# Performance work log

Hardware: AMD Instinct MI355X
Metric: run time of the kernel (lower is better)

Reference implementation:

```python
import jax, jax.numpy as jnp
import numpy as np

N_NODES = 100000
N_EDGES = 1600000
DIM_IN, DIM_H, DIM_OUT = 15, 128, 1


def _glorot(key, shape):
    fan_in, fan_out = shape[0], shape[1]
    lim = float(np.sqrt(6.0 / (fan_in + fan_out)))
    return jax.random.uniform(key, shape, jnp.float32, -lim, lim)


def setup_inputs() -> dict:
    key = jax.random.key(0)
    ks = jax.random.split(key, 12)
    x = jax.random.normal(ks[0], (N_NODES, DIM_IN), jnp.float32)
    edge_index = jax.random.randint(ks[1], (2, N_EDGES), 0, N_NODES, jnp.int64)
    # PyG SAGEConv: out = lin_l(mean_aggr(x_src)) + lin_r(x_dst); bias lives in lin_l.
    # Weights stored as [in, out] for x @ W.
    params = {
        "W1l": _glorot(ks[2], (DIM_IN, DIM_H)), "W1r": _glorot(ks[3], (DIM_IN, DIM_H)), "b1": jnp.zeros((DIM_H,), jnp.float32),
        "W2l": _glorot(ks[4], (DIM_H, DIM_H)), "W2r": _glorot(ks[5], (DIM_H, DIM_H)), "b2": jnp.zeros((DIM_H,), jnp.float32),
        "W3l": _glorot(ks[6], (DIM_H, DIM_OUT)), "W3r": _glorot(ks[7], (DIM_H, DIM_OUT)), "b3": jnp.zeros((DIM_OUT,), jnp.float32),
    }
    return {"x": x, "edge_index": edge_index, **params}


def _sage_conv(h, src, dst, deg_inv, Wl, Wr, b):
    # mean-aggregate source features at destination nodes
    agg = jax.ops.segment_sum(h[src], dst, num_segments=N_NODES) * deg_inv
    return agg @ Wl + h @ Wr + b


def reference(x, edge_index, W1l, W1r, b1, W2l, W2r, b2, W3l, W3r, b3):
    src, dst = edge_index[0], edge_index[1]
    deg = jax.ops.segment_sum(jnp.ones((src.shape[0],), x.dtype), dst, num_segments=N_NODES)
    deg_inv = (1.0 / jnp.maximum(deg, 1.0))[:, None]  # [N,1]
    h = jax.nn.relu(_sage_conv(x, src, dst, deg_inv, W1l, W1r, b1))  # dropout is identity in eval
    h = jax.nn.relu(_sage_conv(h, src, dst, deg_inv, W2l, W2r, b2))
    h = _sage_conv(h, src, dst, deg_inv, W3l, W3r, b3)
    return h
```

## Files before the change

kernel.cpp:

```cpp
#include <hip/hip_runtime.h>
#include <hip/hip_bf16.h>

constexpr int N = 100000;
constexpr int E = 1600000;
constexpr int DIN = 15;
constexpr int DH  = 128;
constexpr int K2  = 256;
constexpr int NPAD = 100032;

constexpr int CHUNK     = 8192;
constexpr int NBLK_P1   = (E + CHUNK - 1) / CHUNK;
constexpr int BKT_NODES = 512;
constexpr int NBKT      = (N + BKT_NODES - 1) / BKT_NODES;
constexpr int LREC_CAP  = 10240;

constexpr int PREP_IDS    = DH * K2 + NPAD * 8 + DH * 32 + (NPAD - N) * 8;
constexpr int PREP_BLOCKS = (PREP_IDS + 1023) / 1024;

typedef short short8 __attribute__((ext_vector_type(8)));
typedef float f32x4  __attribute__((ext_vector_type(4)));

__device__ __forceinline__ unsigned short f2bf_rne(float f) {
    unsigned u = __float_as_uint(f);
    u += 0x7fffu + ((u >> 16) & 1u);
    return (unsigned short)(u >> 16);
}
__device__ __forceinline__ float bf2f(unsigned short h) {
    return __uint_as_float(((unsigned)h) << 16);
}
__device__ __forceinline__ float bflo(unsigned u) { return __uint_as_float(u << 16); }
__device__ __forceinline__ float bfhi(unsigned u) { return __uint_as_float(u & 0xffff0000u); }

__global__ __launch_bounds__(1024) void k_pre(const int* __restrict__ src,
                                              const int* __restrict__ dst,
                                              unsigned int* __restrict__ bsorted,
                                              int* __restrict__ offg,
                                              int* __restrict__ btot,
                                              const float* __restrict__ x,
                                              const float* __restrict__ W2l,
                                              const float* __restrict__ W2r,
                                              const float* __restrict__ W1l,
                                              const float* __restrict__ W1r,
                                              unsigned int* __restrict__ xb32,
                                              unsigned short* __restrict__ Wthi,
                                              unsigned short* __restrict__ Wtlo,
                                              unsigned short* __restrict__ Wt1hi,
                                              unsigned short* __restrict__ Wt1lo,
                                              unsigned int* __restrict__ agg1b) {
    __shared__ int hist[256];
    __shared__ int scn[256];
    __shared__ int fill[256];
    __shared__ unsigned int srt[CHUNK];
    const int t = threadIdx.x;

    if (blockIdx.x >= NBLK_P1) {
        int id = (blockIdx.x - NBLK_P1) * 1024 + t;
        if (id < DH * K2) {
            int col = id & 127;
            int k   = id >> 7;
            float wv = (k < DH) ? W2l[k * DH + col] : W2r[(k - DH) * DH + col];
            unsigned short hi = f2bf_rne(wv);
            unsigned short lo = f2bf_rne(wv - bf2f(hi));
            Wthi[col * K2 + k] = hi;
            Wtlo[col * K2 + k] = lo;
            return;
        }
        int xid = id - DH * K2;
        if (xid < NPAD * 8) {
            int n = xid >> 3, d2 = xid & 7;
            unsigned v = 0;
            if (n < N) {
                int d0 = 2 * d2, d1 = 2 * d2 + 1;
                float v0 = x[n * DIN + d0];
                float v1 = (d1 < DIN) ? x[n * DIN + d1] : 0.f;
                v = (unsigned)f2bf_rne(v0) | ((unsigned)f2bf_rne(v1) << 16);
            }
            xb32[xid] = v;
            return;
        }
        int wid = xid - NPAD * 8;
        if (wid < DH * 32) {
            int col = wid >> 5;
            int k   = wid & 31;
            float wv = 0.f;
            if (k < DIN)                 wv = W1l[k * DH + col];
            else if (k >= 16 && k < 31)  wv = W1r[(k - 16) * DH + col];
            unsigned short hi = f2bf_rne(wv);
            unsigned short lo = f2bf_rne(wv - bf2f(hi));
            Wt1hi[col * 32 + k] = hi;
            Wt1lo[col * 32 + k] = lo;
            return;
        }
        int aid = wid - DH * 32;
        if (aid < (NPAD - N) * 8) agg1b[N * 8 + aid] = 0;
        return;
    }

    const int blk = blockIdx.x;
    const int e0  = blk * CHUNK;
    if (t < 256) hist[t] = 0;
    __syncthreads();
#pragma unroll
    for (int j = 0; j < CHUNK / 1024; ++j) {
        int i = e0 + t + j * 1024;
        if (i < E) atomicAdd(&hist[dst[i] >> 9], 1);
    }
    __syncthreads();
    if (t < 256) {
        if (t < NBKT && hist[t]) atomicAdd(&btot[t], hist[t]);
        scn[t] = hist[t];
    }
    __syncthreads();
    for (int d = 1; d < 256; d <<= 1) {
        int v = (t >= d && t < 256) ? scn[t - d] : 0;
        __syncthreads();
        if (t < 256) scn[t] += v;
        __syncthreads();
    }
    if (t < 256) {
        int excl = (t == 0) ? 0 : scn[t - 1];
        fill[t] = excl;
        if (t < NBKT) offg[blk * (NBKT + 1) + t] = excl;
        if (t == 0)   offg[blk * (NBKT + 1) + NBKT] = scn[NBKT - 1];
    }
    __syncthreads();
#pragma unroll
    for (int j = 0; j < CHUNK / 1024; ++j) {
        int i = e0 + t + j * 1024;
        if (i < E) {
            int dv = dst[i];
            int b  = dv >> 9;
            int pos = atomicAdd(&fill[b], 1);
            srt[pos] = ((unsigned)(dv & 511) << 17) | (unsigned)src[i];
        }
    }
    __syncthreads();
    for (int i = t; i < CHUNK; i += 1024) bsorted[e0 + i] = srt[i];
}

__global__ __launch_bounds__(1024) void k_p2(const unsigned int* __restrict__ bsorted,
                                             const int* __restrict__ offg,
                                             const int* __restrict__ btot,
                                             int* __restrict__ csr,
                                             int* __restrict__ rowptr,
                                             float* __restrict__ deg_inv) {
    __shared__ unsigned int lrec[LREC_CAP];
    __shared__ int cum[NBLK_P1 + 1];
    __shared__ int runstart[NBLK_P1];
    __shared__ int ldeg[BKT_NODES];
    __shared__ int lrp[BKT_NODES];
    __shared__ int lfill[BKT_NODES];
    __shared__ int pscan[256];
    __shared__ int sbs;

    const int b = blockIdx.x;
    const int t = threadIdx.x;

    if (t < 256) pscan[t] = (t < NBKT) ? btot[t] : 0;
    __syncthreads();
    for (int d = 1; d < 256; d <<= 1) {
        int v = (t >= d && t < 256) ? pscan[t - d] : 0;
        __syncthreads();
        if (t < 256) pscan[t] += v;
        __syncthreads();
    }
    if (t == 0) sbs = (b == 0) ? 0 : pscan[b - 1];
    __syncthreads();
    const int bs = sbs;

    int cnt_blk = 0;
    if (t < NBLK_P1) {
        int o0 = offg[t * (NBKT + 1) + b];
        cnt_blk = offg[t * (NBKT + 1) + b + 1] - o0;
        runstart[t] = o0;
    }
    __syncthreads();
    if (t < 256) pscan[t] = cnt_blk;
    __syncthreads();
    for (int d = 1; d < 256; d <<= 1) {
        int v = (t >= d && t < 256) ? pscan[t - d] : 0;
        __syncthreads();
        if (t < 256) pscan[t] += v;
        __syncthreads();
    }
    if (t < NBLK_P1) cum[t] = (t == 0) ? 0 : pscan[t - 1];
    if (t == 0) cum[NBLK_P1] = pscan[NBLK_P1 - 1];
    if (t < BKT_NODES) ldeg[t] = 0;
    __syncthreads();

    int total = cum[NBLK_P1];
    if (total > LREC_CAP) total = LREC_CAP;

    for (int i = t; i < total; i += 1024) {
        int lo = 0, hi = NBLK_P1;
        while (hi - lo > 1) {
            int mid = (lo + hi) >> 1;
            if (cum[mid] <= i) lo = mid; else hi = mid;
        }
        lrec[i] = bsorted[lo * CHUNK + runstart[lo] + (i - cum[lo])];
    }
    __syncthreads();

    for (int i = t; i < total; i += 1024) atomicAdd(&ldeg[lrec[i] >> 17], 1);
    __syncthreads();

    int p0 = 0, p1 = 0;
    if (t < 256) {
        p0 = ldeg[2 * t];
        p1 = ldeg[2 * t + 1];
        pscan[t] = p0 + p1;
    }
    __syncthreads();
    for (int d = 1; d < 256; d <<= 1) {
        int v = (t >= d && t < 256) ? pscan[t - d] : 0;
        __syncthreads();
        if (t < 256) pscan[t] += v;
        __syncthreads();
    }
    if (t < 256) {
        int pairbase = (t == 0) ? 0 : pscan[t - 1];
        lrp[2 * t]     = pairbase;
        lrp[2 * t + 1] = pairbase + p0;
    }
    if (t < BKT_NODES) lfill[t] = 0;
    __syncthreads();

    for (int i = t; i < total; i += 1024) {
        unsigned rec = lrec[i];
        int ld  = rec >> 17;
        int pos = lrp[ld] + atomicAdd(&lfill[ld], 1);
        csr[bs + pos] = (int)(rec & 0x1ffff);
    }
    if (t < BKT_NODES) {
        int g = b * BKT_NODES + t;
        if (g < N) {
            rowptr[g]  = bs + lrp[t];
            deg_inv[g] = 1.0f / fmaxf((float)ldeg[t], 1.0f);
        }
    }
    if (b == NBKT - 1 && t == 0) rowptr[N] = E;
}

__global__ __launch_bounds__(256) void k_agg1(const int* __restrict__ rowptr,
                                              const int* __restrict__ csr,
                                              const uint2* __restrict__ xb2,
                                              const float* __restrict__ deg_inv,
                                              uint2* __restrict__ agg1b2) {
    const int tid = threadIdx.x;
    const int l4  = tid & 3;
    const int gb4 = (tid & 63) & 60;
    const int n = blockIdx.x * 64 + (tid >> 2);
    if (n >= N) return;
    const int lo = rowptr[n], hi = rowptr[n + 1];
    float a0 = 0.f, a1 = 0.f, a2 = 0.f, a3 = 0.f;
    float b0 = 0.f, b1 = 0.f, b2 = 0.f, b3 = 0.f;
    float c0 = 0.f, c1 = 0.f, c2 = 0.f, c3 = 0.f;
    float d0 = 0.f, d1 = 0.f, d2 = 0.f, d3 = 0.f;
    int base = lo;
    for (; base + 8 <= hi; base += 8) {
        int e0 = csr[base + l4];
        int e1 = csr[base + 4 + l4];
        int s0 = __shfl(e0, gb4 + 0), s1 = __shfl(e0, gb4 + 1);
        int s2 = __shfl(e0, gb4 + 2), s3 = __shfl(e0, gb4 + 3);
        int s4 = __shfl(e1, gb4 + 0), s5 = __shfl(e1, gb4 + 1);
        int s6 = __shfl(e1, gb4 + 2), s7 = __shfl(e1, gb4 + 3);
        uint2 u0 = xb2[s0 * 4 + l4];
        uint2 u1 = xb2[s1 * 4 + l4];
        uint2 u2 = xb2[s2 * 4 + l4];
        uint2 u3 = xb2[s3 * 4 + l4];
        uint2 u4 = xb2[s4 * 4 + l4];
        uint2 u5 = xb2[s5 * 4 + l4];
        uint2 u6 = xb2[s6 * 4 + l4];
        uint2 u7 = xb2[s7 * 4 + l4];
        a0 += bflo(u0.x); a1 += bfhi(u0.x); a2 += bflo(u0.y); a3 += bfhi(u0.y);
        b0 += bflo(u1.x); b1 += bfhi(u1.x); b2 += bflo(u1.y); b3 += bfhi(u1.y);
        c0 += bflo(u2.x); c1 += bfhi(u2.x); c2 += bflo(u2.y); c3 += bfhi(u2.y);
        d0 += bflo(u3.x); d1 += bfhi(u3.x); d2 += bflo(u3.y); d3 += bfhi(u3.y);
        a0 += bflo(u4.x); a1 += bfhi(u4.x); a2 += bflo(u4.y); a3 += bfhi(u4.y);
        b0 += bflo(u5.x); b1 += bfhi(u5.x); b2 += bflo(u5.y); b3 += bfhi(u5.y);
        c0 += bflo(u6.x); c1 += bfhi(u6.x); c2 += bflo(u6.y); c3 += bfhi(u6.y);
        d0 += bflo(u7.x); d1 += bfhi(u7.x); d2 += bflo(u7.y); d3 += bfhi(u7.y);
    }
    int cnt = hi - base;
    if (cnt > 0) {
        int e0 = (base + l4 < hi) ? csr[base + l4] : 0;
        int e1 = (base + 4 + l4 < hi) ? csr[base + 4 + l4] : 0;
        int jm = min(cnt, 4);
        for (int j = 0; j < jm; ++j) {
            int s = __shfl(e0, gb4 + j);
            uint2 u = xb2[s * 4 + l4];
            a0 += bflo(u.x); a1 += bfhi(u.x); a2 += bflo(u.y); a3 += bfhi(u.y);
        }
        for (int j = 4; j < cnt; ++j) {
            int s = __shfl(e1, gb4 + j - 4);
            uint2 u = xb2[s * 4 + l4];
            b0 += bflo(u.x); b1 += bfhi(u.x); b2 += bflo(u.y); b3 += bfhi(u.y);
        }
    }
    const float di = deg_inv[n];
    float v0 = ((a0 + b0) + (c0 + d0)) * di;
    float v1 = ((a1 + b1) + (c1 + d1)) * di;
    float v2 = ((a2 + b2) + (c2 + d2)) * di;
    float v3 = ((a3 + b3) + (c3 + d3)) * di;
    uint2 o;
    o.x = (unsigned)f2bf_rne(v0) | ((unsigned)f2bf_rne(v1) << 16);
    o.y = (unsigned)f2bf_rne(v2) | ((unsigned)f2bf_rne(v3) << 16);
    agg1b2[n * 4 + l4] = o;
}

__global__ __launch_bounds__(256) void k_h1(const uint4* __restrict__ agg1b4,
                                            const uint4* __restrict__ xb4,
                                            const unsigned short* __restrict__ Wt1hi,
                                            const unsigned short* __restrict__ Wt1lo,
                                            const float* __restrict__ b1,
                                            unsigned int* __restrict__ h1hi32) {
    __shared__ __align__(16) unsigned short sA[4 * 64 * 8];
    __shared__ __align__(16) unsigned short sH[64 * 128];
    __shared__ float sb[DH];

    const int tid   = threadIdx.x;
    const int node0 = blockIdx.x * 64;

    if (tid < DH) sb[tid] = b1[tid];
    {
        int c = tid >> 6;
        int n = tid & 63;
        uint4 v = (c < 2) ? agg1b4[(node0 + n) * 2 + c]
                          : xb4[(node0 + n) * 2 + (c - 2)];
        *(uint4*)&sA[(c * 64 + (n ^ c)) * 8] = v;
    }
    __syncthreads();

    const int w    = tid >> 6;
    const int lane = tid & 63;
    const int cg   = lane & 15;
    const int lg   = lane >> 4;

    f32x4 acc[4][2];
#pragma unroll
    for (int a = 0; a < 4; ++a)
#pragma unroll
        for (int b = 0; b < 2; ++b)
            acc[a][b] = (f32x4){0.f, 0.f, 0.f, 0.f};

    short8 bh0 = *(const short8*)&Wt1hi[(w * 32 + 0 * 16 + cg) * 32 + lg * 8];
    short8 bh1 = *(const short8*)&Wt1hi[(w * 32 + 1 * 16 + cg) * 32 + lg * 8];
    short8 bl0 = *(const short8*)&Wt1lo[(w * 32 + 0 * 16 + cg) * 32 + lg * 8];
    short8 bl1 = *(const short8*)&Wt1lo[(w * 32 + 1 * 16 + cg) * 32 + lg * 8];

#pragma unroll
    for (int rt = 0; rt < 4; ++rt) {
        const int n = rt * 16 + cg;
        short8 a = *(const short8*)&sA[(lg * 64 + (n ^ lg)) * 8];
        acc[rt][0] = __builtin_amdgcn_mfma_f32_16x16x32_bf16(a, bh0, acc[rt][0], 0, 0, 0);
        acc[rt][0] = __builtin_amdgcn_mfma_f32_16x16x32_bf16(a, bl0, acc[rt][0], 0, 0, 0);
        acc[rt][1] = __builtin_amdgcn_mfma_f32_16x16x32_bf16(a, bh1, acc[rt][1], 0, 0, 0);
        acc[rt][1] = __builtin_amdgcn_mfma_f32_16x16x32_bf16(a, bl1, acc[rt][1], 0, 0, 0);
    }

#pragma unroll
    for (int rt = 0; rt < 4; ++rt)
#pragma unroll
        for (int ci = 0; ci < 2; ++ci) {
            const int col = w * 32 + ci * 16 + cg;
            const float bb = sb[col];
#pragma unroll
            for (int reg = 0; reg < 4; ++reg) {
                const int row = rt * 16 + lg * 4 + reg;
                sH[row * 128 + col] = f2bf_rne(fmaxf(acc[rt][ci][reg] + bb, 0.f));
            }
        }
    __syncthreads();
    const uint4* sH4 = (const uint4*)sH;
    uint4* out4 = (uint4*)h1hi32;
#pragma unroll
    for (int it = 0; it < 4; ++it) {
        int idx = tid + it * 256;
        out4[node0 * 16 + idx] = sH4[idx];
    }
}

__global__ __launch_bounds__(256) void k_agg2(const int* __restrict__ rowptr,
                                              const int* __restrict__ csr,
                                              const unsigned int* __restrict__ h1b,
                                              const float* __restrict__ deg_inv,
                                              unsigned int* __restrict__ agg2b) {
    const int lane = threadIdx.x & 63;
    const int n = blockIdx.x * 4 + (threadIdx.x >> 6);
    if (n >= N) return;
    const int lo = rowptr[n], hi = rowptr[n + 1];
    float a0x = 0.f, a0y = 0.f, a1x = 0.f, a1y = 0.f;
    float a2x = 0.f, a2y = 0.f, a3x = 0.f, a3y = 0.f;
    float a4x = 0.f, a4y = 0.f, a5x = 0.f, a5y = 0.f;
    float a6x = 0.f, a6y = 0.f, a7x = 0.f, a7y = 0.f;
    for (int base = lo; base < hi; base += 64) {
        const int cnt = min(64, hi - base);
        int e = (base + lane < hi) ? csr[base + lane] : 0;
        int j = 0;
        for (; j + 8 <= cnt; j += 8) {
            int s0 = __shfl(e, j + 0), s1 = __shfl(e, j + 1);
            int s2 = __shfl(e, j + 2), s3 = __shfl(e, j + 3);
            int s4 = __shfl(e, j + 4), s5 = __shfl(e, j + 5);
            int s6 = __shfl(e, j + 6), s7 = __shfl(e, j + 7);
            unsigned u0 = h1b[s0 * 64 + lane];
            unsigned u1 = h1b[s1 * 64 + lane];
            unsigned u2 = h1b[s2 * 64 + lane];
            unsigned u3 = h1b[s3 * 64 + lane];
            unsigned u4 = h1b[s4 * 64 + lane];
            unsigned u5 = h1b[s5 * 64 + lane];
            unsigned u6 = h1b[s6 * 64 + lane];
            unsigned u7 = h1b[s7 * 64 + lane];
            a0x += bflo(u0); a0y += bfhi(u0);
            a1x += bflo(u1); a1y += bfhi(u1);
            a2x += bflo(u2); a2y += bfhi(u2);
            a3x += bflo(u3); a3y += bfhi(u3);
            a4x += bflo(u4); a4y += bfhi(u4);
            a5x += bflo(u5); a5y += bfhi(u5);
            a6x += bflo(u6); a6y += bfhi(u6);
            a7x += bflo(u7); a7y += bfhi(u7);
        }
        for (; j < cnt; ++j) {
            int s = __shfl(e, j);
            unsigned u = h1b[s * 64 + lane];
            a0x += bflo(u); a0y += bfhi(u);
        }
    }
    const float di = deg_inv[n];
    float vx = (((a0x + a1x) + (a2x + a3x)) + ((a4x + a5x) + (a6x + a7x))) * di;
    float vy = (((a0y + a1y) + (a2y + a3y)) + ((a4y + a5y) + (a6y + a7y))) * di;
    agg2b[n * 64 + lane] = (unsigned)f2bf_rne(vx) | ((unsigned)f2bf_rne(vy) << 16);
}

__global__ __launch_bounds__(256) void k_h2pr(const unsigned int* __restrict__ agg2b,
                                              const unsigned int* __restrict__ h1hi32,
                                              const unsigned short* __restrict__ Wthi,
                                              const unsigned short* __restrict__ Wtlo,
                                              const float* __restrict__ b2,
                                              const float* __restrict__ W3l,
                                              const float* __restrict__ W3r,
                                              float* __restrict__ p,
                                              float* __restrict__ r) {
    __shared__ __align__(16) unsigned short sA[32 * 64 * 8];
    __shared__ float sb2[DH], sW3l[DH], sW3r[DH];
    __shared__ float sPP[4 * 64], sPR[4 * 64];

    const int tid   = threadIdx.x;
    const int node0 = blockIdx.x * 64;

    if (tid < DH) {
        sb2[tid]  = b2[tid];
        sW3l[tid] = W3l[tid];
        sW3r[tid] = W3r[tid];
    }

#pragma unroll
    for (int it = 0; it < 4; ++it) {
        int idx = tid + it * 256;
        int n   = idx >> 4;
        int cp  = idx & 15;
        uint4 va = *(const uint4*)&agg2b[(node0 + n) * 64 + cp * 4];
        *(uint4*)&sA[(cp * 64 + (n ^ (cp & 7))) * 8] = va;
    }
#pragma unroll
    for (int it = 0; it < 4; ++it) {
        int idx = tid + it * 256;
        int n   = idx >> 4;
        int cp  = idx & 15;
        int c   = 16 + cp;
        uint4 vh = *(const uint4*)&h1hi32[(node0 + n) * 64 + cp * 4];
        *(uint4*)&sA[(c * 64 + (n ^ (cp & 7))) * 8] = vh;
    }
    __syncthreads();

    const int w    = tid >> 6;
    const int lane = tid & 63;
    const int cg   = lane & 15;
    const int lg   = lane >> 4;

    f32x4 acc[4][2];
#pragma unroll
    for (int a = 0; a < 4; ++a)
#pragma unroll
        for (int b = 0; b < 2; ++b)
            acc[a][b] = (f32x4){0.f, 0.f, 0.f, 0.f};

    const unsigned short* bhp0 = &Wthi[(w * 32 + 0 * 16 + cg) * K2 + lg * 8];
    const unsigned short* bhp1 = &Wthi[(w * 32 + 1 * 16 + cg) * K2 + lg * 8];
    const unsigned short* blp0 = &Wtlo[(w * 32 + 0 * 16 + cg) * K2 + lg * 8];
    const unsigned short* blp1 = &Wtlo[(w * 32 + 1 * 16 + cg) * K2 + lg * 8];

#pragma unroll
    for (int s = 0; s < 8; ++s) {
        short8 a[4];
#pragma unroll
        for (int rt = 0; rt < 4; ++rt) {
            const int c = s * 4 + lg;
            const int n = rt * 16 + cg;
            a[rt] = *(const short8*)&sA[(c * 64 + (n ^ (c & 7))) * 8];
        }
        short8 bhi0 = *(const short8*)(bhp0 + s * 32);
        short8 bhi1 = *(const short8*)(bhp1 + s * 32);
        short8 blo0 = *(const short8*)(blp0 + s * 32);
        short8 blo1 = *(const short8*)(blp1 + s * 32);
#pragma unroll
        for (int rt = 0; rt < 4; ++rt) {
            acc[rt][0] = __builtin_amdgcn_mfma_f32_16x16x32_bf16(a[rt], bhi0, acc[rt][0], 0, 0, 0);
            acc[rt][0] = __builtin_amdgcn_mfma_f32_16x16x32_bf16(a[rt], blo0, acc[rt][0], 0, 0, 0);
            acc[rt][1] = __builtin_amdgcn_mfma_f32_16x16x32_bf16(a[rt], bhi1, acc[rt][1], 0, 0, 0);
            acc[rt][1] = __builtin_amdgcn_mfma_f32_16x16x32_bf16(a[rt], blo1, acc[rt][1], 0, 0, 0);
        }
    }

    float pl[4][4] = {{0.f}}, rl[4][4] = {{0.f}};
#pragma unroll
    for (int rt = 0; rt < 4; ++rt)
#pragma unroll
        for (int ci = 0; ci < 2; ++ci) {
            const int col = w * 32 + ci * 16 + cg;
            const float bb = sb2[col], w3l = sW3l[col], w3r = sW3r[col];
#pragma unroll
            for (int reg = 0; reg < 4; ++reg) {
                float h2v = fmaxf(acc[rt][ci][reg] + bb, 0.f);
                pl[rt][reg] = fmaf(h2v, w3l, pl[rt][reg]);
                rl[rt][reg] = fmaf(h2v, w3r, rl[rt][reg]);
            }
        }
#pragma unroll
    for (int m = 8; m >= 1; m >>= 1)
#pragma unroll
        for (int rt = 0; rt < 4; ++rt)
#pragma unroll
            for (int reg = 0; reg < 4; ++reg) {
                pl[rt][reg] += __shfl_xor(pl[rt][reg], m, 64);
                rl[rt][reg] += __shfl_xor(rl[rt][reg], m, 64);
            }
    if (cg == 0) {
#pragma unroll
        for (int rt = 0; rt < 4; ++rt)
#pragma unroll
            for (int reg = 0; reg < 4; ++reg) {
                const int row = rt * 16 + lg * 4 + reg;
                sPP[w * 64 + row] = pl[rt][reg];
                sPR[w * 64 + row] = rl[rt][reg];
            }
    }
    __syncthreads();
    if (tid < 64) {
        float sp = sPP[tid] + sPP[64 + tid] + sPP[128 + tid] + sPP[192 + tid];
        float sr = sPR[tid] + sPR[64 + tid] + sPR[128 + tid] + sPR[192 + tid];
        p[node0 + tid] = sp;
        r[node0 + tid] = sr;
    }
}

__global__ __launch_bounds__(256) void k_out(const int* __restrict__ rowptr,
                                             const int* __restrict__ csr,
                                             const float* __restrict__ p,
                                             const float* __restrict__ r,
                                             const float* __restrict__ deg_inv,
                                             const float* __restrict__ b3,
                                             float* __restrict__ out) {
    const int tid = threadIdx.x;
    const int l7  = tid & 7;
    const int n   = blockIdx.x * 32 + (tid >> 3);
    if (n >= N) return;
    const int lo = rowptr[n], hi = rowptr[n + 1];
    float a = 0.f, b = 0.f;
    int i = lo + l7;
    for (; i + 8 < hi; i += 16) {
        a += p[csr[i]];
        b += p[csr[i + 8]];
    }
    if (i < hi) a += p[csr[i]];
    a += b;
    a += __shfl_xor(a, 1, 64);
    a += __shfl_xor(a, 2, 64);
    a += __shfl_xor(a, 4, 64);
    if (l7 == 0) out[n] = a * deg_inv[n] + r[n] + b3[0];
}

extern "C" void kernel_launch(void* const* d_in, const int* in_sizes, int n_in,
                              void* d_out, int out_size, void* d_ws, size_t ws_size,
                              hipStream_t stream) {
    const float* x    = (const float*)d_in[0];
    const int*   eidx = (const int*)d_in[1];
    const float* W1l  = (const float*)d_in[2];
    const float* W1r  = (const float*)d_in[3];
    const float* b1   = (const float*)d_in[4];
    const float* W2l  = (const float*)d_in[5];
    const float* W2r  = (const float*)d_in[6];
    const float* b2   = (const float*)d_in[7];
    const float* W3l  = (const float*)d_in[8];
    const float* W3r  = (const float*)d_in[9];
    const float* b3   = (const float*)d_in[10];
    float* out = (float*)d_out;

    const int* srcs = eidx;
    const int* dsts = eidx + E;

    size_t off = 0;
    auto alloc = [&](size_t bytes) {
        size_t o = off;
        off = (off + bytes + 255) & ~(size_t)255;
        return o;
    };
    char* w = (char*)d_ws;
    int*   rowptr  = (int*)(w + alloc((size_t)(N + 1) * 4));
    int*   csr     = (int*)(w + alloc((size_t)E * 4));
    float* deg_inv = (float*)(w + alloc((size_t)N * 4));
    unsigned int* xb32   = (unsigned int*)(w + alloc((size_t)NPAD * 8 * 4));
    unsigned int* agg1b  = (unsigned int*)(w + alloc((size_t)NPAD * 8 * 4));
    unsigned short* h1hi = (unsigned short*)(w + alloc((size_t)NPAD * DH * 2));
    unsigned int* agg2b  = (unsigned int*)(w + alloc((size_t)NPAD * 64 * 4));
    float* pbuf    = (float*)(w + alloc((size_t)NPAD * 4));
    float* rbuf    = (float*)(w + alloc((size_t)NPAD * 4));
    unsigned short* Wthi  = (unsigned short*)(w + alloc((size_t)DH * K2 * 2));
    unsigned short* Wtlo  = (unsigned short*)(w + alloc((size_t)DH * K2 * 2));
    unsigned short* Wt1hi = (unsigned short*)(w + alloc((size_t)DH * 32 * 2));
    unsigned short* Wt1lo = (unsigned short*)(w + alloc((size_t)DH * 32 * 2));
    unsigned int* bsorted = (unsigned int*)(w + alloc((size_t)NBLK_P1 * CHUNK * 4));
    int*   offg    = (int*)(w + alloc((size_t)NBLK_P1 * (NBKT + 1) * 4));
    int*   btot    = (int*)(w + alloc((size_t)NBKT * 4));
    (void)ws_size;

    hipMemsetAsync(btot, 0, (size_t)NBKT * 4, stream);
    k_pre<<<NBLK_P1 + PREP_BLOCKS, 1024, 0, stream>>>(srcs, dsts, bsorted, offg, btot,
                                                      x, W2l, W2r, W1l, W1r, xb32,
                                                      Wthi, Wtlo, Wt1hi, Wt1lo, agg1b);
    k_p2<<<NBKT, 1024, 0, stream>>>(bsorted, offg, btot, csr, rowptr, deg_inv);

    k_agg1<<<(N + 63) / 64, 256, 0, stream>>>(rowptr, csr, (const uint2*)xb32,
                                              deg_inv, (uint2*)agg1b);
    k_h1<<<NPAD / 64, 256, 0, stream>>>((const uint4*)agg1b, (const uint4*)xb32,
                                        Wt1hi, Wt1lo, b1, (unsigned int*)h1hi);

    k_agg2<<<(N + 3) / 4, 256, 0, stream>>>(rowptr, csr, (const unsigned int*)h1hi,
                                            deg_inv, agg2b);

    k_h2pr<<<NPAD / 64, 256, 0, stream>>>(agg2b, (const unsigned int*)h1hi,
                                          Wthi, Wtlo, b2, W3l, W3r, pbuf, rbuf);

    k_out<<<(N + 31) / 32, 256, 0, stream>>>(rowptr, csr, pbuf, rbuf, deg_inv, b3, out);
}
```

Before: 172.6 us.

## Split layer-2 aggregation into feature slices with 8 nodes per wavefront

The layer-2 mean aggregation now assigns each 8-lane group one node and one 8-word (16-feature) slice, and launches 8 blocks per node group to cover the 128 features. Each wavefront therefore gathers 8 nodes in parallel instead of one, so the uneven degree of a single node no longer serialises a whole wave. The cost is that neighbor indices are re-read 8 times, once per slice, and each gather is a 32-byte segment rather than a full 256-byte row. Blocks with the same node group and different slices sit next to each other, which may help L2 reuse of the csr entries.

New measurement: 289.1 us. +67.5%, slower.

```diff
diff --git a/kernel.cpp b/kernel.cpp
--- a/kernel.cpp
+++ b/kernel.cpp
@@ -385,50 +385,55 @@
                                               const unsigned int* __restrict__ h1b,
                                               const float* __restrict__ deg_inv,
                                               unsigned int* __restrict__ agg2b) {
-    const int lane = threadIdx.x & 63;
-    const int n = blockIdx.x * 4 + (threadIdx.x >> 6);
+    const int slice = blockIdx.x & 7;
+    const int nblk  = blockIdx.x >> 3;
+    const int lane  = threadIdx.x & 63;
+    const int wv    = threadIdx.x >> 6;
+    const int l8    = lane & 7;
+    const int gb    = lane & 56;
+    const int n = nblk * 32 + wv * 8 + (lane >> 3);
     if (n >= N) return;
+    const int d = slice * 8 + l8;
     const int lo = rowptr[n], hi = rowptr[n + 1];
-    float a0x = 0.f, a0y = 0.f, a1x = 0.f, a1y = 0.f;
-    float a2x = 0.f, a2y = 0.f, a3x = 0.f, a3y = 0.f;
-    float a4x = 0.f, a4y = 0.f, a5x = 0.f, a5y = 0.f;
-    float a6x = 0.f, a6y = 0.f, a7x = 0.f, a7y = 0.f;
-    for (int base = lo; base < hi; base += 64) {
-        const int cnt = min(64, hi - base);
-        int e = (base + lane < hi) ? csr[base + lane] : 0;
-        int j = 0;
-        for (; j + 8 <= cnt; j += 8) {
-            int s0 = __shfl(e, j + 0), s1 = __shfl(e, j + 1);
-            int s2 = __shfl(e, j + 2), s3 = __shfl(e, j + 3);
-            int s4 = __shfl(e, j + 4), s5 = __shfl(e, j + 5);
-            int s6 = __shfl(e, j + 6), s7 = __shfl(e, j + 7);
-            unsigned u0 = h1b[s0 * 64 + lane];
-            unsigned u1 = h1b[s1 * 64 + lane];
-            unsigned u2 = h1b[s2 * 64 + lane];
-            unsigned u3 = h1b[s3 * 64 + lane];
-            unsigned u4 = h1b[s4 * 64 + lane];
-            unsigned u5 = h1b[s5 * 64 + lane];
-            unsigned u6 = h1b[s6 * 64 + lane];
-            unsigned u7 = h1b[s7 * 64 + lane];
-            a0x += bflo(u0); a0y += bfhi(u0);
-            a1x += bflo(u1); a1y += bfhi(u1);
-            a2x += bflo(u2); a2y += bfhi(u2);
-            a3x += bflo(u3); a3y += bfhi(u3);
-            a4x += bflo(u4); a4y += bfhi(u4);
-            a5x += bflo(u5); a5y += bfhi(u5);
-            a6x += bflo(u6); a6y += bfhi(u6);
-            a7x += bflo(u7); a7y += bfhi(u7);
-        }
-        for (; j < cnt; ++j) {
-            int s = __shfl(e, j);
-            unsigned u = h1b[s * 64 + lane];
-            a0x += bflo(u); a0y += bfhi(u);
+    float a0 = 0.f, a1 = 0.f, b0 = 0.f, b1 = 0.f;
+    float c0 = 0.f, c1 = 0.f, d0 = 0.f, d1 = 0.f;
+    int base = lo;
+    for (; base + 8 <= hi; base += 8) {
+        int e = csr[base + l8];
+        int s0 = __shfl(e, gb + 0), s1 = __shfl(e, gb + 1);
+        int s2 = __shfl(e, gb + 2), s3 = __shfl(e, gb + 3);
+        int s4 = __shfl(e, gb + 4), s5 = __shfl(e, gb + 5);
+        int s6 = __shfl(e, gb + 6), s7 = __shfl(e, gb + 7);
+        unsigned u0 = h1b[s0 * 64 + d];
+        unsigned u1 = h1b[s1 * 64 + d];
+        unsigned u2 = h1b[s2 * 64 + d];
+        unsigned u3 = h1b[s3 * 64 + d];
+        unsigned u4 = h1b[s4 * 64 + d];
+        unsigned u5 = h1b[s5 * 64 + d];
+        unsigned u6 = h1b[s6 * 64 + d];
+        unsigned u7 = h1b[s7 * 64 + d];
+        a0 += bflo(u0); a1 += bfhi(u0);
+        b0 += bflo(u1); b1 += bfhi(u1);
+        c0 += bflo(u2); c1 += bfhi(u2);
+        d0 += bflo(u3); d1 += bfhi(u3);
+        a0 += bflo(u4); a1 += bfhi(u4);
+        b0 += bflo(u5); b1 += bfhi(u5);
+        c0 += bflo(u6); c1 += bfhi(u6);
+        d0 += bflo(u7); d1 += bfhi(u7);
+    }
+    int cnt = hi - base;
+    if (cnt > 0) {
+        int e = (base + l8 < hi) ? csr[base + l8] : 0;
+        for (int j = 0; j < cnt; ++j) {
+            int s = __shfl(e, gb + j);
+            unsigned u = h1b[s * 64 + d];
+            a0 += bflo(u); a1 += bfhi(u);
         }
     }
     const float di = deg_inv[n];
-    float vx = (((a0x + a1x) + (a2x + a3x)) + ((a4x + a5x) + (a6x + a7x))) * di;
-    float vy = (((a0y + a1y) + (a2y + a3y)) + ((a4y + a5y) + (a6y + a7y))) * di;
-    agg2b[n * 64 + lane] = (unsigned)f2bf_rne(vx) | ((unsigned)f2bf_rne(vy) << 16);
+    float vx = ((a0 + b0) + (c0 + d0)) * di;
+    float vy = ((a1 + b1) + (c1 + d1)) * di;
+    agg2b[n * 64 + d] = (unsigned)f2bf_rne(vx) | ((unsigned)f2bf_rne(vy) << 16);
 }
 
 __global__ __launch_bounds__(256) void k_h2pr(const unsigned int* __restrict__ agg2b,
@@ -634,8 +639,9 @@
     k_h1<<<NPAD / 64, 256, 0, stream>>>((const uint4*)agg1b, (const uint4*)xb32,
                                         Wt1hi, Wt1lo, b1, (unsigned int*)h1hi);
 
-    k_agg2<<<(N + 3) / 4, 256, 0, stream>>>(rowptr, csr, (const unsigned int*)h1hi,
-                                            deg_inv, agg2b);
+    k_agg2<<<8 * ((N + 31) / 32), 256, 0, stream>>>(rowptr, csr,
+                                                    (const unsigned int*)h1hi,
+                                                    deg_inv, agg2b);
 
     k_h2pr<<<NPAD / 64, 256, 0, stream>>>(agg2b, (const unsigned int*)h1hi,
                                           Wthi, Wtlo, b2, W3l, W3r, pbuf, rbuf);
```
